# Kernel tuning notes

Measured on AMD Instinct MI355X. Metric: run time of the kernel, lower is better.

The kernel has to match this reference:

```python
import jax, jax.numpy as jnp
import numpy as np

B, L, C = 16, 2048, 1024
H, G, K = 16, 4, 5
GC = C // G          # group channels = 256
DH = C // H          # head channels = 64
PAD = K // 2         # 2


def conv1d(x, w, b, pad):
    # x: [N, Cin, L], w: [Cout, Cin, K]
    out = jax.lax.conv_general_dilated(x, w, (1,), [(pad, pad)],
                                       dimension_numbers=('NCH', 'OIH', 'NCH'))
    return out + b[None, :, None]


def setup_inputs() -> dict:
    key = jax.random.key(0)
    ks = jax.random.split(key, 16)
    s = 0.02
    inp = {
        'x': jax.random.normal(ks[0], (B, L, C), jnp.float32),
        'Wq': jax.random.normal(ks[1], (C, C), jnp.float32) * s,
        'bq': jnp.zeros((C,), jnp.float32),
        'Wk': jax.random.normal(ks[2], (C, C), jnp.float32) * s,
        'bk': jnp.zeros((C,), jnp.float32),
        'Wv': jax.random.normal(ks[3], (C, C), jnp.float32) * s,
        'bv': jnp.zeros((C,), jnp.float32),
        'Woff1': jax.random.normal(ks[4], (GC, GC, K), jnp.float32) * s,
        'boff1': jnp.zeros((GC,), jnp.float32),
        'Woff2': jax.random.normal(ks[5], (1, GC, 1), jnp.float32) * s,
        'boff2': jnp.zeros((1,), jnp.float32),
        'rpb_table': jax.random.normal(ks[6], (1, C, L), jnp.float32) * 0.02,
        'Wout': jax.random.normal(ks[7], (C, C), jnp.float32) * s,
        'bout': jnp.zeros((C,), jnp.float32),
    }
    return inp


def reference(x, Wq, bq, Wk, bk, Wv, bv, Woff1, boff1, Woff2, boff2,
              rpb_table, Wout, bout):
    xT = jnp.swapaxes(x, 1, 2)                        # [B, C, L]
    # conv1x1 q projection
    q = jnp.einsum('oc,bcl->bol', Wq, xT) + bq[None, :, None]
    gq = q.reshape(B * G, GC, L)                       # grouped queries
    # offset network: conv(k=5, pad=2) -> conv(k=1, pad=2) => length L+4
    h = conv1d(gq, Woff1, boff1, PAD)                  # [BG, GC, L]
    off = conv1d(h, Woff2, boff2, PAD)                 # [BG, 1, L+4]
    off = jnp.tanh(off[:, 0, :]) * K                   # offset_range_factor = kernel
    L4 = L + 2 * PAD
    grid = jnp.arange(L4, dtype=x.dtype)
    vgrid = grid[None, :] + off                        # [BG, L4]
    vs = 2.0 * vgrid / (L4 - 1) - 1.0                  # normalize with n = L+4 (as in source)
    # grid_sample bilinear, align_corners=False, zeros padding, over length L
    pos = ((vs + 1.0) * L - 1.0) / 2.0
    i0 = jnp.floor(pos)
    w1 = pos - i0
    i0 = i0.astype(jnp.int32)
    feats = xT.reshape(B * G, GC, L)

    def gather(idx):
        valid = ((idx >= 0) & (idx < L)).astype(x.dtype)
        idxc = jnp.clip(idx, 0, L - 1)
        g = jnp.take_along_axis(feats, jnp.broadcast_to(idxc[:, None, :], (B * G, GC, L4)), axis=2)
        return g * valid[:, None, :]

    samp = gather(i0) * (1.0 - w1)[:, None, :] + gather(i0 + 1) * w1[:, None, :]
    x_sampled = samp[:, :, :L].reshape(B, C, L)

    k = jnp.einsum('oc,bcl->bol', Wk, x_sampled) + bk[None, :, None]
    v = jnp.einsum('oc,bcl->bol', Wv, x_sampled) + bv[None, :, None] + rpb_table

    qh = q.reshape(B * H, DH, L)
    kh = k.reshape(B * H, DH, L)
    vh = v.reshape(B * H, DH, L)
    # attention over head-channel dims, contracting over sequence (faithful to source)
    scores = jnp.einsum('bil,bjl->bij', qh, kh) * (C ** -0.5)   # [BH, DH, DH]
    attn = jax.nn.softmax(scores, axis=-1)
    out = jnp.einsum('bij,bjl->bil', attn, vh)                  # [BH, DH, L]
    # rearrange '(b g) l c -> b c (g l)' with b=B, g=H, l=DH, c=L
    out = out.reshape(B, H, DH, L).transpose(0, 3, 1, 2).reshape(B, L, C)
    return out @ Wout.T + bout
```

## Files before the change

kernel.cpp:

```cpp
#include <hip/hip_runtime.h>
#include <hip/hip_bf16.h>
#include <stdint.h>

#define BATCH 16
#define SEQ   2048
#define CH    1024
#define NH    16
#define NG    4
#define KW    5
#define GCH   256
#define DHD   64
#define NBG   (BATCH*NG)
#define NBH   (BATCH*NH)
#define MROWS (BATCH*SEQ)

typedef __hip_bfloat16 bf16;
typedef float f32x4 __attribute__((ext_vector_type(4)));
typedef __bf16 bf16x8 __attribute__((ext_vector_type(8)));

__global__ __launch_bounds__(256)
void cvt_kernel(const float* __restrict__ in, bf16* __restrict__ out, int n)
{
    int i = (blockIdx.x*256 + threadIdx.x)*8;
    if (i >= n) return;
    float4 f0 = *(const float4*)(in+i);
    float4 f1 = *(const float4*)(in+i+4);
    union { bf16 b[8]; uint4 u; } pk;
    pk.b[0]=__float2bfloat16(f0.x); pk.b[1]=__float2bfloat16(f0.y);
    pk.b[2]=__float2bfloat16(f0.z); pk.b[3]=__float2bfloat16(f0.w);
    pk.b[4]=__float2bfloat16(f1.x); pk.b[5]=__float2bfloat16(f1.y);
    pk.b[6]=__float2bfloat16(f1.z); pk.b[7]=__float2bfloat16(f1.w);
    *(uint4*)(out+i) = pk.u;
}

__global__ void prep_weff_kernel(const float* __restrict__ W1, const float* __restrict__ b1,
                                 const float* __restrict__ w2, const float* __restrict__ b2,
                                 float* __restrict__ weff, float* __restrict__ wcst)
{
    int kk = blockIdx.x;
    int cj = threadIdx.x;
    float s = 0.f;
    for (int co=0; co<GCH; ++co)
        s += w2[co] * W1[((size_t)co*GCH + cj)*KW + kk];
    weff[kk*GCH + cj] = s;
    if (kk==0 && cj==0){
        float sb = 0.f;
        for (int co=0; co<GCH; ++co) sb += w2[co]*b1[co];
        wcst[0] = b2[0];
        wcst[1] = sb;
    }
}

template<int MODE>
__global__ __launch_bounds__(512, 2)
void gemm256_kernel(const bf16* __restrict__ A, const bf16* __restrict__ Wb,
                    const float* __restrict__ bias, const float* __restrict__ rpb,
                    void* __restrict__ outp)
{
    __shared__ __bf16 SM[3*16384];
    const int t = threadIdx.x;
    const int w = t>>6, l = t&63;
    const int wrow = w>>2, wcol = w&3;
    const int lr = l&15, kslot = l>>4;

    const int lin = blockIdx.x;
    const int xcd = lin&7, sblk = lin>>3;
    const int m0 = (xcd*16 + (sblk>>2))*256;
    const int n0 = (sblk&3)*256;

    const bf16* Ag = A  + (size_t)m0*CH;
    const bf16* Bg = Wb + (size_t)n0*CH;

    int srow[2], scol[2];
    #pragma unroll
    for (int r=0;r<2;++r){
        int o = (t + 512*r)*16;
        int e = o ^ (((o>>7)&3)<<4);
        srow[r] = e>>6;
        scol[r] = (e&63)>>1;
    }

    auto STAGE = [&](int tile, int buf){
        const int kt = tile*32;
        __bf16* ab = SM + buf*16384;
        __bf16* bb = ab + 8192;
        #pragma unroll
        for (int r=0;r<2;++r){
            __builtin_amdgcn_global_load_lds(
                (const __attribute__((address_space(1))) void*)(Ag + (size_t)srow[r]*CH + kt + scol[r]),
                (__attribute__((address_space(3))) void*)(ab + w*512 + r*4096), 16, 0, 0);
            __builtin_amdgcn_global_load_lds(
                (const __attribute__((address_space(1))) void*)(Bg + (size_t)srow[r]*CH + kt + scol[r]),
                (__attribute__((address_space(3))) void*)(bb + w*512 + r*4096), 16, 0, 0);
        }
    };

    f32x4 acc[8][4];
    #pragma unroll
    for (int i=0;i<8;++i)
        #pragma unroll
        for (int j=0;j<4;++j) acc[i][j] = (f32x4){0.f,0.f,0.f,0.f};

    STAGE(0, 0);
    STAGE(1, 1);
    STAGE(2, 2);

    const int NT = CH/32;
    for (int tt=0; tt<NT; ++tt){
        const int cur = tt%3;
        const int rem = NT-1 - tt;
        if (rem >= 2)      asm volatile("s_waitcnt vmcnt(8)" ::: "memory");
        else if (rem == 1) asm volatile("s_waitcnt vmcnt(4)" ::: "memory");
        else               asm volatile("s_waitcnt vmcnt(0)" ::: "memory");
        __builtin_amdgcn_s_barrier();

        const __bf16* As_ = SM + cur*16384;
        const __bf16* Bs_ = As_ + 8192;
        bf16x8 af[8], bfr[4];
        #pragma unroll
        for (int fi=0; fi<8; ++fi){
            int row = wrow*128 + fi*16 + lr;
            int o = row*64 + kslot*16;
            o ^= ((o>>7)&3)<<4;
            af[fi] = *(const bf16x8*)(As_ + (o>>1));
        }
        #pragma unroll
        for (int fj=0; fj<4; ++fj){
            int row = wcol*64 + fj*16 + lr;
            int o = row*64 + kslot*16;
            o ^= ((o>>7)&3)<<4;
            bfr[fj] = *(const bf16x8*)(Bs_ + (o>>1));
        }
        asm volatile("s_waitcnt lgkmcnt(0)" ::: "memory");
        __builtin_amdgcn_s_barrier();

        if (tt+3 < NT) STAGE(tt+3, cur);

        __builtin_amdgcn_s_setprio(1);
        #pragma unroll
        for (int fi=0; fi<8; ++fi)
            #pragma unroll
            for (int fj=0; fj<4; ++fj)
                acc[fi][fj] = __builtin_amdgcn_mfma_f32_16x16x32_bf16(af[fi], bfr[fj], acc[fi][fj], 0,0,0);
        __builtin_amdgcn_s_setprio(0);
    }

    float bs[4];
    #pragma unroll
    for (int fj=0;fj<4;++fj) bs[fj] = bias[n0 + wcol*64 + fj*16 + lr];

    if constexpr (MODE == 2){
        const int bb2 = m0 >> 11;
        const int l0g = m0 & (SEQ-1);
        bf16* outT = (bf16*)outp;
        #pragma unroll
        for (int fi=0; fi<8; ++fi){
            int rowl = wrow*128 + fi*16 + kslot*4;
            #pragma unroll
            for (int fj=0; fj<4; ++fj){
                int col = n0 + wcol*64 + fj*16 + lr;
                union { bf16 h[4]; uint2 u; } pk;
                #pragma unroll
                for (int r=0;r<4;++r) pk.h[r] = __float2bfloat16(acc[fi][fj][r] + bs[fj]);
                *(uint2*)(outT + ((size_t)(bb2*CH + col))*SEQ + l0g + rowl) = pk.u;
            }
        }
    } else {
        #pragma unroll
        for (int fi=0; fi<8; ++fi){
            #pragma unroll
            for (int r=0;r<4;++r){
                int mg = m0 + wrow*128 + fi*16 + kslot*4 + r;
                int lseq = mg & (SEQ-1);
                #pragma unroll
                for (int fj=0; fj<4; ++fj){
                    int ng = n0 + wcol*64 + fj*16 + lr;
                    float v = acc[fi][fj][r] + bs[fj];
                    if constexpr (MODE==1) v += rpb[(size_t)ng*SEQ + lseq];
                    if constexpr (MODE==3)
                        ((float*)outp)[(size_t)mg*CH + ng] = v;
                    else
                        ((bf16*)outp)[(size_t)mg*CH + ng] = __float2bfloat16(v);
                }
            }
        }
    }
}

__global__ __launch_bounds__(256)
void offsets_kernel(const bf16* __restrict__ QT, const float* __restrict__ weff,
                    const float* __restrict__ wcst, float* __restrict__ posb)
{
    __shared__ float P5L[264][5];
    __shared__ float weffL[KW][GCH];
    const int t = threadIdx.x;
    const int chunk = blockIdx.x, bg = blockIdx.y;
    const int b = bg>>2, g = bg&3;
    const int l0 = chunk*256;

    for (int i = t; i < KW*GCH; i += 256) weffL[i/GCH][i&(GCH-1)] = weff[i];
    __syncthreads();

    for (int idx = t; idx < 260; idx += 256){
        int j = l0 - 4 + idx;
        float a0=0.f,a1=0.f,a2=0.f,a3=0.f,a4=0.f;
        if (j >= 0 && j < SEQ){
            const bf16* src = QT + ((size_t)(b*CH + g*GCH))*SEQ + j;
            #pragma unroll 4
            for (int ch=0; ch<GCH; ++ch){
                float v = __bfloat162float(src[(size_t)ch*SEQ]);
                a0 += v*weffL[0][ch]; a1 += v*weffL[1][ch]; a2 += v*weffL[2][ch];
                a3 += v*weffL[3][ch]; a4 += v*weffL[4][ch];
            }
        }
        P5L[idx][0]=a0; P5L[idx][1]=a1; P5L[idx][2]=a2; P5L[idx][3]=a3; P5L[idx][4]=a4;
    }
    __syncthreads();

    int lp = l0 + t;
    float b2 = wcst[0], wb1 = wcst[1];
    float o;
    if (lp < 2){
        o = b2;
    } else {
        float s = b2 + wb1;
        #pragma unroll
        for (int kk=0;kk<KW;++kk){
            int j = lp - 4 + kk;
            if (j >= 0 && j < SEQ) s += P5L[t+kk][kk];
        }
        o = s;
    }
    float off = tanhf(o) * (float)KW;
    posb[bg*SEQ + lp] = ((float)lp + off) * (2048.0f/2051.0f) - 0.5f;
}

__global__ __launch_bounds__(256)
void sample_kernel(const bf16* __restrict__ Xbf, const float* __restrict__ posb,
                   bf16* __restrict__ XS)
{
    const int ci = threadIdx.x, bg = blockIdx.y;
    const int b = bg>>2, g = bg&3;
    const int lp0 = blockIdx.x*8;
    #pragma unroll
    for (int s8=0; s8<8; ++s8){
        int lp = lp0 + s8;
        float p  = posb[bg*SEQ + lp];
        float fl = floorf(p);
        float w1 = p - fl;
        int i0 = (int)fl;
        float v = 0.f;
        if (i0 >= 0 && i0 < SEQ)
            v += __bfloat162float(Xbf[((size_t)(b*SEQ + i0))*CH + g*GCH + ci]) * (1.f - w1);
        if (i0+1 >= 0 && i0+1 < SEQ)
            v += __bfloat162float(Xbf[((size_t)(b*SEQ + i0 + 1))*CH + g*GCH + ci]) * w1;
        XS[((size_t)(b*SEQ + lp))*CH + g*GCH + ci] = __float2bfloat16(v);
    }
}

__global__ __launch_bounds__(256)
void attn_s_kernel(const bf16* __restrict__ QT, const bf16* __restrict__ KT,
                   bf16* __restrict__ Pbuf)
{
    __shared__ float Sc[64][69];
    __shared__ float red[64][4];
    __shared__ float mrow[64];
    __shared__ float sinv[64];
    const int t = threadIdx.x, w = t>>6, l = t&63;
    const int bh = blockIdx.x, b = bh>>4, h = bh&15;
    const bf16* q = QT + ((size_t)(b*CH + h*DHD))*SEQ;
    const bf16* k = KT + ((size_t)(b*CH + h*DHD))*SEQ;
    const int lr = l&15, lk = (l>>4)*8;

    f32x4 acc[4][4];
    #pragma unroll
    for (int i=0;i<4;++i)
        #pragma unroll
        for (int j=0;j<4;++j) acc[i][j] = (f32x4){0.f,0.f,0.f,0.f};

    for (int ks=0; ks<16; ++ks){
        int kp = w*512 + ks*32 + lk;
        bf16x8 af[4], bk8[4];
        #pragma unroll
        for (int i=0;i<4;++i) af[i]  = *(const bf16x8*)(q + (size_t)(i*16+lr)*SEQ + kp);
        #pragma unroll
        for (int j=0;j<4;++j) bk8[j] = *(const bf16x8*)(k + (size_t)(j*16+lr)*SEQ + kp);
        #pragma unroll
        for (int i=0;i<4;++i)
            #pragma unroll
            for (int j=0;j<4;++j)
                acc[i][j] = __builtin_amdgcn_mfma_f32_16x16x32_bf16(af[i], bk8[j], acc[i][j], 0,0,0);
    }
    for (int wv=0; wv<4; ++wv){
        if (w == wv){
            #pragma unroll
            for (int i=0;i<4;++i)
                #pragma unroll
                for (int j=0;j<4;++j)
                    #pragma unroll
                    for (int r=0;r<4;++r){
                        int m = i*16 + (l>>4)*4 + r, n = j*16 + lr;
                        if (wv==0) Sc[m][n]  = acc[i][j][r];
                        else       Sc[m][n] += acc[i][j][r];
                    }
        }
        __syncthreads();
    }
    const int r0 = t & 63, p = t >> 6;
    const float SCALE = 0.03125f;
    float mx = -1e30f;
    #pragma unroll
    for (int c=0;c<16;++c) mx = fmaxf(mx, Sc[r0][p*16+c]*SCALE);
    red[r0][p] = mx;
    __syncthreads();
    if (t < 64) mrow[t] = fmaxf(fmaxf(red[t][0],red[t][1]), fmaxf(red[t][2],red[t][3]));
    __syncthreads();
    float m = mrow[r0], s = 0.f;
    #pragma unroll
    for (int c=0;c<16;++c){
        float e = expf(Sc[r0][p*16+c]*SCALE - m);
        Sc[r0][p*16+c] = e;
        s += e;
    }
    red[r0][p] = s;
    __syncthreads();
    if (t < 64) sinv[t] = 1.f/(red[t][0]+red[t][1]+red[t][2]+red[t][3]);
    __syncthreads();
    float inv = sinv[r0];
    union { bf16 b[8]; uint4 u; } p0, p1;
    #pragma unroll
    for (int e=0;e<8;++e){
        p0.b[e] = __float2bfloat16(Sc[r0][p*16+e]*inv);
        p1.b[e] = __float2bfloat16(Sc[r0][p*16+8+e]*inv);
    }
    bf16* dst = Pbuf + (size_t)bh*4096 + r0*64 + p*16;
    *(uint4*)dst       = p0.u;
    *(uint4*)(dst + 8) = p1.u;
}

__global__ __launch_bounds__(256)
void attn_pv_kernel(const bf16* __restrict__ Pbuf, const bf16* __restrict__ V,
                    bf16* __restrict__ F)
{
    __shared__ __bf16 Pl[64][72];
    const int t = threadIdx.x, w = t>>6, l = t&63;
    const int chunk = blockIdx.x, bh = blockIdx.y;
    const int b = bh>>4, h = bh&15;
    {
        int row = t>>2, coff = (t&3)*16;
        const bf16* src = Pbuf + (size_t)bh*4096 + row*64 + coff;
        *(uint4*)&Pl[row][coff]   = *(const uint4*)src;
        *(uint4*)&Pl[row][coff+8] = *(const uint4*)(src+8);
    }
    __syncthreads();
    const int lr = l&15, lk = (l>>4)*8;
    const int lw = chunk*256 + w*64;

    f32x4 acc[4][4];
    #pragma unroll
    for (int i=0;i<4;++i)
        #pragma unroll
        for (int j=0;j<4;++j) acc[i][j] = (f32x4){0.f,0.f,0.f,0.f};

    #pragma unroll
    for (int ks=0; ks<2; ++ks){
        bf16x8 pf[4], vf[4];
        #pragma unroll
        for (int ni=0;ni<4;++ni) pf[ni] = *(const bf16x8*)&Pl[ni*16+lr][ks*32+lk];
        #pragma unroll
        for (int mi=0;mi<4;++mi)
            vf[mi] = *(const bf16x8*)(V + ((size_t)(b*SEQ + lw + mi*16 + lr))*CH + h*DHD + ks*32 + lk);
        #pragma unroll
        for (int mi=0;mi<4;++mi)
            #pragma unroll
            for (int ni=0;ni<4;++ni)
                acc[mi][ni] = __builtin_amdgcn_mfma_f32_16x16x32_bf16(vf[mi], pf[ni], acc[mi][ni], 0,0,0);
    }
    #pragma unroll
    for (int mi=0;mi<4;++mi){
        #pragma unroll
        for (int r=0;r<4;++r){
            int lpos = lw + mi*16 + (l>>4)*4 + r;
            #pragma unroll
            for (int ni=0;ni<4;++ni)
                F[((size_t)(b*SEQ + lpos))*CH + h*DHD + ni*16 + lr] =
                    __float2bfloat16(acc[mi][ni][r]);
        }
    }
}

extern "C" void kernel_launch(void* const* d_in, const int* in_sizes, int n_in,
                              void* d_out, int out_size, void* d_ws, size_t ws_size,
                              hipStream_t stream)
{
    const float* x   = (const float*)d_in[0];
    const float* Wq  = (const float*)d_in[1];
    const float* bq  = (const float*)d_in[2];
    const float* Wk  = (const float*)d_in[3];
    const float* bk  = (const float*)d_in[4];
    const float* Wv  = (const float*)d_in[5];
    const float* bv  = (const float*)d_in[6];
    const float* W1  = (const float*)d_in[7];
    const float* b1  = (const float*)d_in[8];
    const float* w2  = (const float*)d_in[9];
    const float* b2  = (const float*)d_in[10];
    const float* rpb = (const float*)d_in[11];
    const float* Wo  = (const float*)d_in[12];
    const float* bo  = (const float*)d_in[13];

    char* ws = (char*)d_ws;
    bf16*  Xbf  = (bf16*)(ws);
    bf16*  QT   = (bf16*)(ws + (size_t) 67108864);
    bf16*  XS   = (bf16*)(ws + (size_t)134217728);
    bf16*  VB   = (bf16*)(ws + (size_t)201326592);
    bf16*  Pbuf = (bf16*)(ws + (size_t)268435456);
    bf16*  wslot= (bf16*)(ws + (size_t)270532608);
    float* posb = (float*)(ws + (size_t)272629760);
    float* weff = (float*)(ws + (size_t)273154048);
    float* wcst = (float*)(ws + (size_t)273159168);
    bf16*  KT = Xbf;
    bf16*  Fb = XS;

    prep_weff_kernel<<<dim3(KW), dim3(GCH), 0, stream>>>(W1, b1, w2, b2, weff, wcst);
    cvt_kernel<<<dim3(MROWS*CH/8/256), 256, 0, stream>>>(x, Xbf, MROWS*CH);

    cvt_kernel<<<dim3(CH*CH/8/256), 256, 0, stream>>>(Wq, wslot, CH*CH);
    gemm256_kernel<2><<<dim3(512), 512, 0, stream>>>(Xbf, wslot, bq, nullptr, QT);

    offsets_kernel<<<dim3(SEQ/256, NBG), 256, 0, stream>>>(QT, weff, wcst, posb);
    sample_kernel<<<dim3(SEQ/8, NBG), 256, 0, stream>>>(Xbf, posb, XS);

    cvt_kernel<<<dim3(CH*CH/8/256), 256, 0, stream>>>(Wk, wslot, CH*CH);
    gemm256_kernel<2><<<dim3(512), 512, 0, stream>>>(XS, wslot, bk, nullptr, KT);

    cvt_kernel<<<dim3(CH*CH/8/256), 256, 0, stream>>>(Wv, wslot, CH*CH);
    gemm256_kernel<1><<<dim3(512), 512, 0, stream>>>(XS, wslot, bv, rpb, VB);

    attn_s_kernel<<<dim3(NBH), 256, 0, stream>>>(QT, KT, Pbuf);
    attn_pv_kernel<<<dim3(8, NBH), 256, 0, stream>>>(Pbuf, VB, Fb);

    cvt_kernel<<<dim3(CH*CH/8/256), 256, 0, stream>>>(Wo, wslot, CH*CH);
    gemm256_kernel<3><<<dim3(512), 512, 0, stream>>>(Fb, wslot, bo, nullptr, (float*)d_out);
}
```

Before: 647.1 us.

## Restructure GEMM LDS pipeline to single barrier and flatten offsets conv loop

```diff
diff --git a/kernel.cpp b/kernel.cpp
--- a/kernel.cpp
+++ b/kernel.cpp
@@ -103,16 +103,15 @@
 
     STAGE(0, 0);
     STAGE(1, 1);
-    STAGE(2, 2);
+    asm volatile("s_waitcnt vmcnt(4)" ::: "memory");
+    __builtin_amdgcn_s_barrier();
+    __builtin_amdgcn_sched_barrier(0);
 
     const int NT = CH/32;
     for (int tt=0; tt<NT; ++tt){
         const int cur = tt%3;
-        const int rem = NT-1 - tt;
-        if (rem >= 2)      asm volatile("s_waitcnt vmcnt(8)" ::: "memory");
-        else if (rem == 1) asm volatile("s_waitcnt vmcnt(4)" ::: "memory");
-        else               asm volatile("s_waitcnt vmcnt(0)" ::: "memory");
-        __builtin_amdgcn_s_barrier();
+        if (tt+2 < NT) STAGE(tt+2, (tt+2)%3);
+        __builtin_amdgcn_sched_barrier(0);
 
         const __bf16* As_ = SM + cur*16384;
         const __bf16* Bs_ = As_ + 8192;
@@ -132,9 +131,7 @@
             bfr[fj] = *(const bf16x8*)(Bs_ + (o>>1));
         }
         asm volatile("s_waitcnt lgkmcnt(0)" ::: "memory");
-        __builtin_amdgcn_s_barrier();
-
-        if (tt+3 < NT) STAGE(tt+3, cur);
+        __builtin_amdgcn_sched_barrier(0);
 
         __builtin_amdgcn_s_setprio(1);
         #pragma unroll
@@ -143,6 +140,11 @@
             for (int fj=0; fj<4; ++fj)
                 acc[fi][fj] = __builtin_amdgcn_mfma_f32_16x16x32_bf16(af[fi], bfr[fj], acc[fi][fj], 0,0,0);
         __builtin_amdgcn_s_setprio(0);
+
+        if (tt+2 < NT)      asm volatile("s_waitcnt vmcnt(4)" ::: "memory");
+        else                asm volatile("s_waitcnt vmcnt(0)" ::: "memory");
+        __builtin_amdgcn_s_barrier();
+        __builtin_amdgcn_sched_barrier(0);
     }
 
     float bs[4];
@@ -201,19 +203,29 @@
     for (int i = t; i < KW*GCH; i += 256) weffL[i/GCH][i&(GCH-1)] = weff[i];
     __syncthreads();
 
-    for (int idx = t; idx < 260; idx += 256){
-        int j = l0 - 4 + idx;
-        float a0=0.f,a1=0.f,a2=0.f,a3=0.f,a4=0.f;
-        if (j >= 0 && j < SEQ){
-            const bf16* src = QT + ((size_t)(b*CH + g*GCH))*SEQ + j;
-            #pragma unroll 4
-            for (int ch=0; ch<GCH; ++ch){
-                float v = __bfloat162float(src[(size_t)ch*SEQ]);
-                a0 += v*weffL[0][ch]; a1 += v*weffL[1][ch]; a2 += v*weffL[2][ch];
-                a3 += v*weffL[3][ch]; a4 += v*weffL[4][ch];
-            }
-        }
-        P5L[idx][0]=a0; P5L[idx][1]=a1; P5L[idx][2]=a2; P5L[idx][3]=a3; P5L[idx][4]=a4;
+    const int j1 = l0 - 4 + t;
+    const int j2 = l0 + 252 + t;
+    const bool v1 = (j1 >= 0) & (j1 < SEQ);
+    const bool v2 = (t < 4);
+    float a1[KW] = {0,0,0,0,0};
+    float a2[KW] = {0,0,0,0,0};
+    const bf16* src = QT + ((size_t)(b*CH + g*GCH))*SEQ;
+    for (int ch=0; ch<GCH; ++ch){
+        const bf16* row = src + (size_t)ch*SEQ;
+        float x1 = v1 ? __bfloat162float(row[j1 & (SEQ-1)]) : 0.f;
+        #pragma unroll
+        for (int kk=0;kk<KW;++kk) a1[kk] += x1*weffL[kk][ch];
+        if (v2){
+            float x2 = __bfloat162float(row[j2]);
+            #pragma unroll
+            for (int kk=0;kk<KW;++kk) a2[kk] += x2*weffL[kk][ch];
+        }
+    }
+    #pragma unroll
+    for (int kk=0;kk<KW;++kk) P5L[t][kk] = a1[kk];
+    if (t < 4){
+        #pragma unroll
+        for (int kk=0;kk<KW;++kk) P5L[256+t][kk] = a2[kk];
     }
     __syncthreads();
 
```

Result: slower. 725.7 us (+12.2%).
